# Kernel tuning notes

Measured on AMD Instinct MI355X. Metric: run time of the kernel, lower is better.

The kernel has to match this reference:

```python
import jax, jax.numpy as jnp
import numpy as np

STRIDE = 1
KSIZE = 3
DEMOD = True


def _conv_single(xi, wi, pad):
    # xi: [C,H,W], wi: [O,C,k,k] -> [O,H,W]
    out = jax.lax.conv_general_dilated(
        xi[None], wi, window_strides=(STRIDE, STRIDE),
        padding=[(pad, pad), (pad, pad)],
        dimension_numbers=("NCHW", "OIHW", "NCHW"))
    return out[0]


def setup_inputs() -> dict:
    key = jax.random.key(0)
    ks = jax.random.split(key, 6)
    B, Cin, Cout, S, H, W = 8, 512, 512, 512, 64, 64
    return {
        "x": jax.random.normal(ks[0], (B, Cin, H, W), jnp.float32),
        "y": jax.random.normal(ks[1], (B, S), jnp.float32),
        "affine_w": jax.random.normal(ks[2], (Cin, S), jnp.float32) * 0.02,
        "affine_b": jax.random.normal(ks[3], (Cin,), jnp.float32) * 0.02,
        "weight": jax.random.normal(ks[4], (Cout, Cin, KSIZE, KSIZE), jnp.float32) * 0.05,
        "bias": jax.random.normal(ks[5], (1, Cout, 1, 1), jnp.float32) * 0.02,
    }


def reference(x, y, affine_w, affine_b, weight, bias):
    B, _, H, W = x.shape
    style_dim = affine_w.shape[1]
    coef = 1.0 / np.sqrt(style_dim)  # ELR: gain / sqrt(fan_in)
    # style modulation scale per input channel: [B, Cin]
    s = (y * coef) @ affine_w.T + affine_b + 1.0
    # per-sample weights: [B, O, I, k, k]
    w = weight[None, :, :, :, :] * s[:, None, :, None, None]
    if DEMOD:
        d = jax.lax.rsqrt(jnp.sum(w * w, axis=(2, 3, 4), keepdims=True) + 1e-4)
        w = w * d
    pad = ((H - 1) * (STRIDE - 1) + (KSIZE - 1)) // 2
    out = jax.vmap(lambda xi, wi: _conv_single(xi, wi, pad))(x, w)  # [B,O,H,W]
    return out + bias
```

## Files before the change

kernel.cpp:

```cpp
#include <hip/hip_runtime.h>

typedef __attribute__((ext_vector_type(8))) short short8;
typedef __attribute__((ext_vector_type(4))) float floatx4;
typedef unsigned short u16;
typedef unsigned int u32;

#define NB 8
#define CI 512
#define CO 512
#define HH 64
#define WW 64
#define HP 66
#define WP 66
#define BK 64

__device__ __forceinline__ u16 f2bf(float f) {
  u32 u = __builtin_bit_cast(u32, f);
  u += 0x7fffu + ((u >> 16) & 1u);
  return (u16)(u >> 16);
}

__device__ __forceinline__ void gload16(const void* g, void* l) {
  __builtin_amdgcn_global_load_lds(
      (const __attribute__((address_space(1))) unsigned int*)g,
      (__attribute__((address_space(3))) unsigned int*)l, 16, 0, 0);
}

__global__ __launch_bounds__(256) void k_style(
    const float* __restrict__ y, const float* __restrict__ aw,
    const float* __restrict__ ab, float* __restrict__ s)
{
  const int wid = blockIdx.x * 4 + (threadIdx.x >> 6);
  const int lane = threadIdx.x & 63;
  const int b = wid >> 9, i = wid & 511;
  float sum = 0.f;
  #pragma unroll
  for (int j = 0; j < 8; ++j) {
    const int k = lane + (j << 6);
    sum += y[b * CI + k] * aw[i * CI + k];
  }
  #pragma unroll
  for (int off = 32; off; off >>= 1) sum += __shfl_xor(sum, off);
  if (lane == 0) s[wid] = sum * 0.044194173824159216f + ab[i] + 1.0f;
}

__global__ __launch_bounds__(256) void k_wprep(
    const float* __restrict__ wt, float* __restrict__ wsum, u16* __restrict__ wbv)
{
  const int idx = blockIdx.x * 256 + threadIdx.x;
  const int i = idx & 511;
  const int o = idx >> 9;
  const float* p = wt + (size_t)idx * 9;
  float v[9];
  float sum = 0.f;
  #pragma unroll
  for (int t = 0; t < 9; ++t) { v[t] = p[t]; sum += v[t] * v[t]; }
  wsum[idx] = sum;
  #pragma unroll
  for (int t = 0; t < 9; ++t) wbv[(((o * 9 + t) << 9) | i)] = f2bf(v[t]);
}

__global__ __launch_bounds__(256) void k_demod(
    const float* __restrict__ wsum, const float* __restrict__ s,
    float* __restrict__ d)
{
  const int wid = blockIdx.x * 4 + (threadIdx.x >> 6);
  const int lane = threadIdx.x & 63;
  const int b = wid >> 9, o = wid & 511;
  float sum = 0.f;
  #pragma unroll
  for (int j = 0; j < 8; ++j) {
    const int i = lane + (j << 6);
    const float sv = s[b * CI + i];
    sum += wsum[o * CI + i] * sv * sv;
  }
  #pragma unroll
  for (int off = 32; off; off >>= 1) sum += __shfl_xor(sum, off);
  if (lane == 0) d[wid] = rsqrtf(sum + 1e-4f);
}

__global__ __launch_bounds__(256) void k_xform(
    const float* __restrict__ x, const float* __restrict__ s,
    u16* __restrict__ xs)
{
  __shared__ __align__(16) u16 lds[64 * 72];
  const int blk = blockIdx.x;
  const int ic = blk & 7;
  const int h = (blk >> 3) & 63;
  const int b = blk >> 9;
  const int i0 = ic << 6;
  const int t = threadIdx.x;
  const int w = t & 63;
  const int i4 = t >> 6;
  #pragma unroll
  for (int p = 0; p < 16; ++p) {
    const int ii = i4 + (p << 2);
    const float xv = x[((size_t)(b * CI + i0 + ii) * HH + h) * WW + w];
    const float sv = s[b * CI + i0 + ii];
    lds[w * 72 + ii] = f2bf(xv * sv);
  }
  const uint4 z4 = {0u, 0u, 0u, 0u};
  if (t < 16) {
    const int wside = (t < 8) ? 0 : 65;
    const int q = t & 7;
    *(uint4*)&xs[((size_t)(b * HP + h + 1) * WP + wside) * CI + i0 + (q << 3)] = z4;
  }
  if (h == 0) {
    for (int idx = t; idx < 2 * 66 * 8; idx += 256) {
      const int row = (idx < 528) ? 0 : 65;
      const int rem = (idx < 528) ? idx : idx - 528;
      const int wz = rem >> 3;
      const int q = rem & 7;
      *(uint4*)&xs[((size_t)(b * HP + row) * WP + wz) * CI + i0 + (q << 3)] = z4;
    }
  }
  __syncthreads();
  const int w2 = t >> 2;
  const int q = t & 3;
  const uint4* src = (const uint4*)&lds[w2 * 72 + (q << 4)];
  const uint4 v0 = src[0];
  const uint4 v1 = src[1];
  u16* dst = xs + ((size_t)(b * HP + h + 1) * WP + (w2 + 1)) * CI + i0 + (q << 4);
  *(uint4*)dst = v0;
  *((uint4*)dst + 1) = v1;
}

__global__ __launch_bounds__(512, 2) void k_conv(
    const u16* __restrict__ xs, const u16* __restrict__ wb,
    const float* __restrict__ dmod, const float* __restrict__ bias,
    float* __restrict__ out)
{
  __shared__ __align__(16) u16 lA[2 * 16384];
  __shared__ __align__(16) u16 lB[2 * 16384];

  const int blk = blockIdx.x;
  const int nt = blk & 15;
  const int mt = (blk >> 4) & 1;
  const int b  = blk >> 5;
  const int ob = mt << 8;
  const int p0 = nt << 8;

  const int tid = threadIdx.x;
  const int wid = tid >> 6;
  const int lane = tid & 63;
  const int col = lane & 15;
  const int k8  = lane >> 4;
  const int wr  = wid >> 2;
  const int wc  = wid & 3;

  const int lr = lane >> 3;
  const int ls = lane & 7;
  const int swz = ls ^ lr;

  u32 aoff[4], boff[4], ldst[4];
  #pragma unroll
  for (int h2 = 0; h2 < 4; ++h2) {
    const int rowBase = ((h2 >> 1) << 7) + (wid << 4) + ((h2 & 1) << 3);
    const int rowIdx = rowBase + lr;
    aoff[h2] = (u32)((ob + rowIdx) * 4608 + (swz << 3));
    const int p = p0 + rowIdx;
    boff[h2] = (u32)(((b * HP + (p >> 6)) * WP + (p & 63)) * 512 + (swz << 3));
    ldst[h2] = (u32)(rowBase << 6);
  }

  const u32 sA0 = (u32)(((0 + k8) ^ (col & 7)) << 3);
  const u32 sA1 = (u32)(((4 + k8) ^ (col & 7)) << 3);
  const u32 aRead = (u32)((((wr << 7) + col) << 6));
  const u32 bRead = (u32)((((wc << 6) + col) << 6));

  floatx4 acc[8][4];
  #pragma unroll
  for (int m = 0; m < 8; ++m)
    #pragma unroll
    for (int n = 0; n < 4; ++n)
      acc[m][n] = (floatx4){0.f, 0.f, 0.f, 0.f};

  short8 a0[4][2], b0[2][2], b1[2][2];

#define SA(TILE, H, BUF) do {                                                 \
    const u32 at_ = (u32)((TILE) << 6);                                       \
    gload16(wb + aoff[(H)*2+0] + at_, &lA[((BUF) << 14) + ldst[(H)*2+0]]);    \
    gload16(wb + aoff[(H)*2+1] + at_, &lA[((BUF) << 14) + ldst[(H)*2+1]]);    \
  } while (0)

#define SB(TILE, H, BUF) do {                                                 \
    const int t_ = (TILE);                                                    \
    const int tap_ = t_ >> 3;                                                 \
    const int kh_ = tap_ / 3;                                                 \
    const int kw_ = tap_ - kh_ * 3;                                           \
    const u32 bt_ = (u32)(((kh_ * WP + kw_) << 9) + ((t_ & 7) << 6));         \
    gload16(xs + boff[(H)*2+0] + bt_, &lB[((BUF) << 14) + ldst[(H)*2+0]]);    \
    gload16(xs + boff[(H)*2+1] + bt_, &lB[((BUF) << 14) + ldst[(H)*2+1]]);    \
  } while (0)

#define READ_A(PA, MH) do {                                                   \
    _Pragma("unroll")                                                         \
    for (int mq = 0; mq < 4; ++mq) {                                          \
      a0[mq][0] = *(const short8*)((PA) + (MH) * 4096 + mq * 1024 + sA0);     \
      a0[mq][1] = *(const short8*)((PA) + (MH) * 4096 + mq * 1024 + sA1);     \
    }                                                                         \
  } while (0)

#define READ_B(PB, NH, BV) do {                                               \
    _Pragma("unroll")                                                         \
    for (int nq = 0; nq < 2; ++nq) {                                          \
      BV[nq][0] = *(const short8*)((PB) + (NH) * 2048 + nq * 1024 + sA0);     \
      BV[nq][1] = *(const short8*)((PB) + (NH) * 2048 + nq * 1024 + sA1);     \
    }                                                                         \
  } while (0)

#define MFMA_Q(MH, NH, BV) do {                                               \
    _Pragma("unroll")                                                         \
    for (int kk = 0; kk < 2; ++kk)                                            \
      _Pragma("unroll")                                                       \
      for (int nq = 0; nq < 2; ++nq)                                          \
        _Pragma("unroll")                                                     \
        for (int mq = 0; mq < 4; ++mq)                                        \
          acc[(MH)*4+mq][(NH)*2+nq] = __builtin_amdgcn_mfma_f32_16x16x32_bf16(\
              a0[mq][kk], BV[nq][kk], acc[(MH)*4+mq][(NH)*2+nq], 0, 0, 0);    \
  } while (0)

#define SBAR __builtin_amdgcn_s_barrier()
#define SCH0 __builtin_amdgcn_sched_barrier(0)
#define PRI1 __builtin_amdgcn_s_setprio(1)
#define PRI0 __builtin_amdgcn_s_setprio(0)

#define BODY8(T0, FULL) do {                                                  \
    const u16* pA0 = lA + aRead;                                              \
    const u16* pB0 = lB + bRead;                                              \
    const u16* pA1 = lA + 16384 + aRead;                                      \
    const u16* pB1 = lB + 16384 + bRead;                                      \
                                        \
    READ_A(pA0, 0); READ_B(pB0, 0, b0);                                       \
    SCH0; SA((T0) + 1, 0, 1);                                                 \
    SBAR; PRI1; MFMA_Q(0, 0, b0); PRI0; SBAR;                                 \
                                                          \
    READ_B(pB0, 1, b1);                                                       \
    SCH0; SA((T0) + 1, 1, 1);                                                 \
    SBAR; PRI1; MFMA_Q(0, 1, b1); PRI0; SBAR;                                 \
                           \
    READ_A(pA0, 1);                                                           \
    SCH0; if (FULL) SB((T0) + 2, 0, 0);                                       \
    SBAR; PRI1; MFMA_Q(1, 1, b1); PRI0; SBAR;                                 \
                          \
    SCH0; if (FULL) SB((T0) + 2, 1, 0);                                       \
    SBAR; PRI1; MFMA_Q(1, 0, b0); PRI0;                                       \
    if (FULL) asm volatile("s_waitcnt vmcnt(4)" ::: "memory");                \
    else      asm volatile("s_waitcnt vmcnt(0)" ::: "memory");                \
    SBAR;                                                                     \
       \
    READ_A(pA1, 0); READ_B(pB1, 0, b0);                                       \
    SCH0; if (FULL) SA((T0) + 2, 0, 0);                                       \
    SBAR; PRI1; MFMA_Q(0, 0, b0); PRI0; SBAR;                                 \
                                                          \
    READ_B(pB1, 1, b1);                                                       \
    SCH0; if (FULL) SA((T0) + 2, 1, 0);                                       \
    SBAR; PRI1; MFMA_Q(0, 1, b1); PRI0; SBAR;                                 \
                           \
    READ_A(pA1, 1);                                                           \
    SCH0; if (FULL) SB((T0) + 3, 0, 1);                                       \
    SBAR; PRI1; MFMA_Q(1, 1, b1); PRI0; SBAR;                                 \
                          \
    SCH0; if (FULL) SB((T0) + 3, 1, 1);                                       \
    SBAR; PRI1; MFMA_Q(1, 0, b0); PRI0;                                       \
    if (FULL) asm volatile("s_waitcnt vmcnt(4)" ::: "memory");                \
    SBAR;                                                                     \
  } while (0)

  SB(0, 0, 0); SB(0, 1, 0); SA(0, 0, 0); SA(0, 1, 0);
  SB(1, 0, 1); SB(1, 1, 1);
  asm volatile("s_waitcnt vmcnt(4)" ::: "memory");
  SCH0;
  SBAR;

  for (int j = 0; j < 35; ++j) BODY8(j * 2, 1);
  BODY8(70, 0);

#undef SA
#undef SB
#undef READ_A
#undef READ_B
#undef MFMA_Q
#undef BODY8
#undef SBAR
#undef SCH0
#undef PRI1
#undef PRI0

  #pragma unroll
  for (int m = 0; m < 8; ++m) {
    #pragma unroll
    for (int r = 0; r < 4; ++r) {
      const int o = ob + (wr << 7) + (m << 4) + (k8 << 2) + r;
      const float dm = dmod[b * CO + o];
      const float bs = bias[o];
      float* po = out + (((size_t)(b * CO + o)) << 12) + p0 + (wc << 6);
      #pragma unroll
      for (int n = 0; n < 4; ++n)
        po[(n << 4) + col] = acc[m][n][r] * dm + bs;
    }
  }
}

extern "C" void kernel_launch(void* const* d_in, const int* in_sizes, int n_in,
                              void* d_out, int out_size, void* d_ws, size_t ws_size,
                              hipStream_t stream) {
  const float* x    = (const float*)d_in[0];
  const float* y    = (const float*)d_in[1];
  const float* aw   = (const float*)d_in[2];
  const float* ab   = (const float*)d_in[3];
  const float* wt   = (const float*)d_in[4];
  const float* bias = (const float*)d_in[5];
  float* out = (float*)d_out;

  char* ws = (char*)d_ws;
  const size_t XS_BYTES = (size_t)NB * HP * WP * CI * 2;
  const size_t WB_BYTES = (size_t)CO * 9 * CI * 2;
  const size_t WS_BYTES = (size_t)CO * CI * 4;
  u16* xsb    = (u16*)ws;
  u16* wbuf   = (u16*)(ws + XS_BYTES);
  float* wsum = (float*)(ws + XS_BYTES + WB_BYTES);
  float* sbuf = (float*)(ws + XS_BYTES + WB_BYTES + WS_BYTES);
  float* dbuf = sbuf + NB * CI;

  k_style<<<dim3(1024), dim3(256), 0, stream>>>(y, aw, ab, sbuf);
  k_wprep<<<dim3(1024), dim3(256), 0, stream>>>(wt, wsum, wbuf);
  k_demod<<<dim3(1024), dim3(256), 0, stream>>>(wsum, sbuf, dbuf);
  k_xform<<<dim3(4096), dim3(256), 0, stream>>>(x, sbuf, xsb);
  k_conv <<<dim3(256), dim3(512), 0, stream>>>(xsb, wbuf, dbuf, bias, out);
}
```

Before: 157.4 us.

## Restructure main loop into register double-buffered ping-pong with fewer barriers

Replaces the eight-phase barrier-heavy loop body with a per-tile schedule. A-fragment reads are split into quarter sets that alternate between two register sets, and the next tile's B fragments are prefetched from LDS while the last MFMAs run. Each tile now uses two barriers instead of eight, and global-to-LDS staging is issued in full four-load groups after a vmcnt(0) wait. This aims to cut barrier stalls and hide LDS latency, at the cost of more live registers and a coarser vmcnt wait that may expose global load latency.

```diff
diff --git a/kernel.cpp b/kernel.cpp
--- a/kernel.cpp
+++ b/kernel.cpp
@@ -175,115 +175,110 @@
     for (int n = 0; n < 4; ++n)
       acc[m][n] = (floatx4){0.f, 0.f, 0.f, 0.f};
 
-  short8 a0[4][2], b0[2][2], b1[2][2];
-
-#define SA(TILE, H, BUF) do {                                                 \
-    const u32 at_ = (u32)((TILE) << 6);                                       \
-    gload16(wb + aoff[(H)*2+0] + at_, &lA[((BUF) << 14) + ldst[(H)*2+0]]);    \
-    gload16(wb + aoff[(H)*2+1] + at_, &lA[((BUF) << 14) + ldst[(H)*2+1]]);    \
-  } while (0)
-
-#define SB(TILE, H, BUF) do {                                                 \
-    const int t_ = (TILE);                                                    \
+  short8 setA[2][2], setB[2][2], b0[2][2], b1[2][2];
+
+#define STAGE_A(T, BUF) do {                                                  \
+    const u32 at_ = (u32)((T) << 6);                                          \
+    _Pragma("unroll")                                                         \
+    for (int g = 0; g < 4; ++g)                                               \
+      gload16(wb + aoff[g] + at_, &lA[((BUF) << 14) + ldst[g]]);              \
+  } while (0)
+
+#define STAGE_B(T, BUF) do {                                                  \
+    const int t_ = (T);                                                       \
     const int tap_ = t_ >> 3;                                                 \
     const int kh_ = tap_ / 3;                                                 \
     const int kw_ = tap_ - kh_ * 3;                                           \
     const u32 bt_ = (u32)(((kh_ * WP + kw_) << 9) + ((t_ & 7) << 6));         \
-    gload16(xs + boff[(H)*2+0] + bt_, &lB[((BUF) << 14) + ldst[(H)*2+0]]);    \
-    gload16(xs + boff[(H)*2+1] + bt_, &lB[((BUF) << 14) + ldst[(H)*2+1]]);    \
-  } while (0)
-
-#define READ_A(PA, MH) do {                                                   \
-    _Pragma("unroll")                                                         \
-    for (int mq = 0; mq < 4; ++mq) {                                          \
-      a0[mq][0] = *(const short8*)((PA) + (MH) * 4096 + mq * 1024 + sA0);     \
-      a0[mq][1] = *(const short8*)((PA) + (MH) * 4096 + mq * 1024 + sA1);     \
+    _Pragma("unroll")                                                         \
+    for (int g = 0; g < 4; ++g)                                               \
+      gload16(xs + boff[g] + bt_, &lB[((BUF) << 14) + ldst[g]]);              \
+  } while (0)
+
+#define READ_Q(SET, PA, Q) do {                                               \
+    _Pragma("unroll")                                                         \
+    for (int mq2 = 0; mq2 < 2; ++mq2) {                                       \
+      SET[mq2][0] = *(const short8*)((PA) + ((Q)*2+mq2) * 1024 + sA0);        \
+      SET[mq2][1] = *(const short8*)((PA) + ((Q)*2+mq2) * 1024 + sA1);        \
     }                                                                         \
   } while (0)
 
-#define READ_B(PB, NH, BV) do {                                               \
-    _Pragma("unroll")                                                         \
-    for (int nq = 0; nq < 2; ++nq) {                                          \
-      BV[nq][0] = *(const short8*)((PB) + (NH) * 2048 + nq * 1024 + sA0);     \
-      BV[nq][1] = *(const short8*)((PB) + (NH) * 2048 + nq * 1024 + sA1);     \
+#define READ_BH(BV, PB, NH) do {                                              \
+    _Pragma("unroll")                                                         \
+    for (int nq2 = 0; nq2 < 2; ++nq2) {                                       \
+      BV[nq2][0] = *(const short8*)((PB) + (NH) * 2048 + nq2 * 1024 + sA0);   \
+      BV[nq2][1] = *(const short8*)((PB) + (NH) * 2048 + nq2 * 1024 + sA1);   \
     }                                                                         \
   } while (0)
 
-#define MFMA_Q(MH, NH, BV) do {                                               \
+#define MFMA_P(Q, NH, ASET, BV) do {                                          \
     _Pragma("unroll")                                                         \
     for (int kk = 0; kk < 2; ++kk)                                            \
       _Pragma("unroll")                                                       \
-      for (int nq = 0; nq < 2; ++nq)                                          \
+      for (int nq2 = 0; nq2 < 2; ++nq2)                                       \
         _Pragma("unroll")                                                     \
-        for (int mq = 0; mq < 4; ++mq)                                        \
-          acc[(MH)*4+mq][(NH)*2+nq] = __builtin_amdgcn_mfma_f32_16x16x32_bf16(\
-              a0[mq][kk], BV[nq][kk], acc[(MH)*4+mq][(NH)*2+nq], 0, 0, 0);    \
+        for (int mq2 = 0; mq2 < 2; ++mq2)                                     \
+          acc[(Q)*2+mq2][(NH)*2+nq2] = __builtin_amdgcn_mfma_f32_16x16x32_bf16(\
+              ASET[mq2][kk], BV[nq2][kk], acc[(Q)*2+mq2][(NH)*2+nq2], 0,0,0); \
   } while (0)
 
 #define SBAR __builtin_amdgcn_s_barrier()
-#define SCH0 __builtin_amdgcn_sched_barrier(0)
 #define PRI1 __builtin_amdgcn_s_setprio(1)
 #define PRI0 __builtin_amdgcn_s_setprio(0)
 
-#define BODY8(T0, FULL) do {                                                  \
-    const u16* pA0 = lA + aRead;                                              \
-    const u16* pB0 = lB + bRead;                                              \
-    const u16* pA1 = lA + 16384 + aRead;                                      \
-    const u16* pB1 = lB + 16384 + bRead;                                      \
-                                        \
-    READ_A(pA0, 0); READ_B(pB0, 0, b0);                                       \
-    SCH0; SA((T0) + 1, 0, 1);                                                 \
-    SBAR; PRI1; MFMA_Q(0, 0, b0); PRI0; SBAR;                                 \
-                                                          \
-    READ_B(pB0, 1, b1);                                                       \
-    SCH0; SA((T0) + 1, 1, 1);                                                 \
-    SBAR; PRI1; MFMA_Q(0, 1, b1); PRI0; SBAR;                                 \
-                           \
-    READ_A(pA0, 1);                                                           \
-    SCH0; if (FULL) SB((T0) + 2, 0, 0);                                       \
-    SBAR; PRI1; MFMA_Q(1, 1, b1); PRI0; SBAR;                                 \
-                          \
-    SCH0; if (FULL) SB((T0) + 2, 1, 0);                                       \
-    SBAR; PRI1; MFMA_Q(1, 0, b0); PRI0;                                       \
-    if (FULL) asm volatile("s_waitcnt vmcnt(4)" ::: "memory");                \
-    else      asm volatile("s_waitcnt vmcnt(0)" ::: "memory");                \
+#define TILE8(T, C, FULL) do {                                                \
+    const u16* pA  = lA + ((C) << 14) + aRead;                                \
+    const u16* pA1 = lA + ((1 - (C)) << 14) + aRead;                          \
+    const u16* pB1 = lB + ((1 - (C)) << 14) + bRead;                          \
+     READ_Q(setB, pA, 1);                                            \
+    PRI1; MFMA_P(0, 0, setA, b0); PRI0;                                       \
+     PRI1; MFMA_P(0, 1, setA, b1); PRI0;                             \
+     READ_Q(setA, pA, 2);                                            \
+    PRI1; MFMA_P(1, 0, setB, b0); PRI0;                                       \
+     PRI1; MFMA_P(1, 1, setB, b1); PRI0;                             \
+     READ_Q(setB, pA, 3);                                            \
+    PRI1; MFMA_P(2, 0, setA, b0); PRI0;                                       \
+     PRI1; MFMA_P(2, 1, setA, b1); PRI0;                             \
+    asm volatile("s_waitcnt vmcnt(0)" ::: "memory");                          \
     SBAR;                                                                     \
-       \
-    READ_A(pA1, 0); READ_B(pB1, 0, b0);                                       \
-    SCH0; if (FULL) SA((T0) + 2, 0, 0);                                       \
-    SBAR; PRI1; MFMA_Q(0, 0, b0); PRI0; SBAR;                                 \
-                                                          \
-    READ_B(pB1, 1, b1);                                                       \
-    SCH0; if (FULL) SA((T0) + 2, 1, 0);                                       \
-    SBAR; PRI1; MFMA_Q(0, 1, b1); PRI0; SBAR;                                 \
-                           \
-    READ_A(pA1, 1);                                                           \
-    SCH0; if (FULL) SB((T0) + 3, 0, 1);                                       \
-    SBAR; PRI1; MFMA_Q(1, 1, b1); PRI0; SBAR;                                 \
-                          \
-    SCH0; if (FULL) SB((T0) + 3, 1, 1);                                       \
-    SBAR; PRI1; MFMA_Q(1, 0, b0); PRI0;                                       \
-    if (FULL) asm volatile("s_waitcnt vmcnt(4)" ::: "memory");                \
+         \
+    if (FULL) STAGE_B((T) + 2, C);                                            \
+    READ_Q(setA, pA1, 0);                                                     \
+    PRI1; MFMA_P(3, 0, setB, b0); PRI0;                                       \
+    READ_BH(b0, pB1, 0);                  \
     SBAR;                                                                     \
-  } while (0)
-
-  SB(0, 0, 0); SB(0, 1, 0); SA(0, 0, 0); SA(0, 1, 0);
-  SB(1, 0, 1); SB(1, 1, 1);
-  asm volatile("s_waitcnt vmcnt(4)" ::: "memory");
-  SCH0;
+                                                                     \
+    if (FULL) STAGE_A((T) + 2, C);                                            \
+    PRI1; MFMA_P(3, 1, setB, b1); PRI0;                                       \
+    READ_BH(b1, pB1, 1);                               \
+  } while (0)
+
+  STAGE_B(0, 0); STAGE_A(0, 0);
+  STAGE_B(1, 1); STAGE_A(1, 1);
+  asm volatile("s_waitcnt vmcnt(8)" ::: "memory");
   SBAR;
-
-  for (int j = 0; j < 35; ++j) BODY8(j * 2, 1);
-  BODY8(70, 0);
-
-#undef SA
-#undef SB
-#undef READ_A
-#undef READ_B
-#undef MFMA_Q
-#undef BODY8
+  {
+    const u16* pA0 = lA + aRead;
+    const u16* pB0 = lB + bRead;
+    READ_Q(setA, pA0, 0);
+    READ_BH(b0, pB0, 0);
+    READ_BH(b1, pB0, 1);
+  }
+
+  for (int j = 0; j < 35; ++j) {
+    TILE8(2 * j,     0, 1);
+    TILE8(2 * j + 1, 1, 1);
+  }
+  TILE8(70, 0, 0);
+  TILE8(71, 1, 0);
+
+#undef STAGE_A
+#undef STAGE_B
+#undef READ_Q
+#undef READ_BH
+#undef MFMA_P
+#undef TILE8
 #undef SBAR
-#undef SCH0
 #undef PRI1
 #undef PRI0
 
```

After: 166.5 us. 1.06x slower.

## Merge prep kernels into two launches and remap conv block order for XCD locality

Applied to the files above, without the earlier changes.

Combines style and weight-prep into one launch and demod with the input transform into another, using block-index ranges to pick the branch, so five launches become three. The conv grid is also remapped so that consecutive block IDs, which are distributed round-robin across the chip's 8 dies (XCDs), group blocks by batch and output tile, with the aim of improving L2 reuse of weights and activations. The merges remove launch gaps and the serialization between independent prep stages, at the cost of heterogeneous blocks within a single kernel.

```diff
diff --git a/kernel.cpp b/kernel.cpp
--- a/kernel.cpp
+++ b/kernel.cpp
@@ -26,64 +26,62 @@
       (__attribute__((address_space(3))) unsigned int*)l, 16, 0, 0);
 }
 
-__global__ __launch_bounds__(256) void k_style(
+__global__ __launch_bounds__(256) void k_prep1(
     const float* __restrict__ y, const float* __restrict__ aw,
-    const float* __restrict__ ab, float* __restrict__ s)
+    const float* __restrict__ ab, float* __restrict__ s,
+    const float* __restrict__ wt, float* __restrict__ wsum,
+    u16* __restrict__ wbv)
 {
-  const int wid = blockIdx.x * 4 + (threadIdx.x >> 6);
-  const int lane = threadIdx.x & 63;
-  const int b = wid >> 9, i = wid & 511;
-  float sum = 0.f;
-  #pragma unroll
-  for (int j = 0; j < 8; ++j) {
-    const int k = lane + (j << 6);
-    sum += y[b * CI + k] * aw[i * CI + k];
-  }
-  #pragma unroll
-  for (int off = 32; off; off >>= 1) sum += __shfl_xor(sum, off);
-  if (lane == 0) s[wid] = sum * 0.044194173824159216f + ab[i] + 1.0f;
-}
-
-__global__ __launch_bounds__(256) void k_wprep(
-    const float* __restrict__ wt, float* __restrict__ wsum, u16* __restrict__ wbv)
-{
-  const int idx = blockIdx.x * 256 + threadIdx.x;
-  const int i = idx & 511;
-  const int o = idx >> 9;
-  const float* p = wt + (size_t)idx * 9;
-  float v[9];
-  float sum = 0.f;
-  #pragma unroll
-  for (int t = 0; t < 9; ++t) { v[t] = p[t]; sum += v[t] * v[t]; }
-  wsum[idx] = sum;
-  #pragma unroll
-  for (int t = 0; t < 9; ++t) wbv[(((o * 9 + t) << 9) | i)] = f2bf(v[t]);
-}
-
-__global__ __launch_bounds__(256) void k_demod(
-    const float* __restrict__ wsum, const float* __restrict__ s,
+  if (blockIdx.x < 1024) {
+    const int wid = blockIdx.x * 4 + (threadIdx.x >> 6);
+    const int lane = threadIdx.x & 63;
+    const int b = wid >> 9, i = wid & 511;
+    float sum = 0.f;
+    #pragma unroll
+    for (int j = 0; j < 8; ++j) {
+      const int k = lane + (j << 6);
+      sum += y[b * CI + k] * aw[i * CI + k];
+    }
+    #pragma unroll
+    for (int off = 32; off; off >>= 1) sum += __shfl_xor(sum, off);
+    if (lane == 0) s[wid] = sum * 0.044194173824159216f + ab[i] + 1.0f;
+  } else {
+    const int idx = (blockIdx.x - 1024) * 256 + threadIdx.x;
+    const int i = idx & 511;
+    const int o = idx >> 9;
+    const float* p = wt + (size_t)idx * 9;
+    float v[9];
+    float sum = 0.f;
+    #pragma unroll
+    for (int t = 0; t < 9; ++t) { v[t] = p[t]; sum += v[t] * v[t]; }
+    wsum[idx] = sum;
+    #pragma unroll
+    for (int t = 0; t < 9; ++t) wbv[(((o * 9 + t) << 9) | i)] = f2bf(v[t]);
+  }
+}
+
+__global__ __launch_bounds__(256) void k_xfd(
+    const float* __restrict__ x, const float* __restrict__ s,
+    u16* __restrict__ xs, const float* __restrict__ wsum,
     float* __restrict__ d)
 {
-  const int wid = blockIdx.x * 4 + (threadIdx.x >> 6);
-  const int lane = threadIdx.x & 63;
-  const int b = wid >> 9, o = wid & 511;
-  float sum = 0.f;
-  #pragma unroll
-  for (int j = 0; j < 8; ++j) {
-    const int i = lane + (j << 6);
-    const float sv = s[b * CI + i];
-    sum += wsum[o * CI + i] * sv * sv;
-  }
-  #pragma unroll
-  for (int off = 32; off; off >>= 1) sum += __shfl_xor(sum, off);
-  if (lane == 0) d[wid] = rsqrtf(sum + 1e-4f);
-}
-
-__global__ __launch_bounds__(256) void k_xform(
-    const float* __restrict__ x, const float* __restrict__ s,
-    u16* __restrict__ xs)
-{
   __shared__ __align__(16) u16 lds[64 * 72];
+  if (blockIdx.x >= 4096) {
+    const int wid = (blockIdx.x - 4096) * 4 + (threadIdx.x >> 6);
+    const int lane = threadIdx.x & 63;
+    const int b = wid >> 9, o = wid & 511;
+    float sum = 0.f;
+    #pragma unroll
+    for (int j = 0; j < 8; ++j) {
+      const int i = lane + (j << 6);
+      const float sv = s[b * CI + i];
+      sum += wsum[o * CI + i] * sv * sv;
+    }
+    #pragma unroll
+    for (int off = 32; off; off >>= 1) sum += __shfl_xor(sum, off);
+    if (lane == 0) d[wid] = rsqrtf(sum + 1e-4f);
+    return;
+  }
   const int blk = blockIdx.x;
   const int ic = blk & 7;
   const int h = (blk >> 3) & 63;
@@ -133,10 +131,11 @@
   __shared__ __align__(16) u16 lA[2 * 16384];
   __shared__ __align__(16) u16 lB[2 * 16384];
 
-  const int blk = blockIdx.x;
-  const int nt = blk & 15;
-  const int mt = (blk >> 4) & 1;
-  const int b  = blk >> 5;
+  const int blk0 = blockIdx.x;
+  const int lblk = ((blk0 & 7) << 5) + (blk0 >> 3);
+  const int mt = lblk >> 7;
+  const int b  = (lblk >> 4) & 7;
+  const int nt = lblk & 15;
   const int ob = mt << 8;
   const int p0 = nt << 8;
 
@@ -323,9 +322,7 @@
   float* sbuf = (float*)(ws + XS_BYTES + WB_BYTES + WS_BYTES);
   float* dbuf = sbuf + NB * CI;
 
-  k_style<<<dim3(1024), dim3(256), 0, stream>>>(y, aw, ab, sbuf);
-  k_wprep<<<dim3(1024), dim3(256), 0, stream>>>(wt, wsum, wbuf);
-  k_demod<<<dim3(1024), dim3(256), 0, stream>>>(wsum, sbuf, dbuf);
-  k_xform<<<dim3(4096), dim3(256), 0, stream>>>(x, sbuf, xsb);
+  k_prep1<<<dim3(2048), dim3(256), 0, stream>>>(y, aw, ab, sbuf, wt, wsum, wbuf);
+  k_xfd  <<<dim3(5120), dim3(256), 0, stream>>>(x, sbuf, xsb, wsum, dbuf);
   k_conv <<<dim3(256), dim3(512), 0, stream>>>(xsb, wbuf, dbuf, bias, out);
 }
```

Measured after the change: 158.9 us. Within noise of the previous version (+0.9%).
